# Optimization experiments

Measured on AMD Instinct MI355X. Metric: run time of the kernel, lower is better.

The kernel has to match this reference:

```python
import jax, jax.numpy as jnp
import numpy as np

EPS = 1e-5
LEAKY = 0.2


def _wn(v, g):
    # weight norm over all dims except output-channel dim 0 (torch default dim=0)
    return g * v / jnp.sqrt(jnp.sum(v * v, axis=(1, 2), keepdims=True))


def _conv1d(x_bsc, w, b):
    # x_bsc: [B,S,C_in]; w: [C_out,C_in,3]; kernel 3, stride 1, pad 1
    x = x_bsc.transpose(0, 2, 1)  # NCH
    y = jax.lax.conv_general_dilated(x, w, (1,), [(1, 1)],
                                     dimension_numbers=("NCH", "OIH", "NCH"))
    y = y + b[None, :, None]
    return y.transpose(0, 2, 1)


def _adain(x, style, lengths, proj_w, proj_b):
    # masked per-(sample,channel) instance norm over valid length, then style affine, then mask
    B, S, H = x.shape
    hs = style @ proj_w.T + proj_b            # [B, 2H]
    gamma, beta = hs[:, :H], hs[:, H:]
    mask = (jnp.arange(S)[None, :] < lengths[:, None]).astype(x.dtype)[..., None]  # [B,S,1]
    cnt = lengths.astype(x.dtype)[:, None, None]
    mean = jnp.sum(x * mask, axis=1, keepdims=True) / cnt
    var = jnp.sum(jnp.square(x - mean) * mask, axis=1, keepdims=True) / cnt  # biased, as F.instance_norm
    xn = (x - mean) * jax.lax.rsqrt(var + EPS)
    out = ((1.0 + gamma[:, None, :]) * xn + beta[:, None, :]) * mask
    return out, mask


def setup_inputs() -> dict:
    key = jax.random.key(0)
    ks = jax.random.split(key, 12)
    B, S, H, STY = 8, 2048, 512, 128
    inp = {
        "hidden_states": jax.random.normal(ks[0], (B, S, H), jnp.float32),
        "style": jax.random.normal(ks[1], (B, STY), jnp.float32),
        "input_lengths": jax.random.randint(ks[2], (B,), S // 2, S + 1, jnp.int32),
        # AdaIN projections (torch Linear: [out,in])
        "proj1_w": jax.random.normal(ks[3], (2 * H, STY), jnp.float32) * 0.02,
        "proj1_b": jnp.zeros((2 * H,), jnp.float32),
        "proj2_w": jax.random.normal(ks[4], (2 * H, STY), jnp.float32) * 0.02,
        "proj2_b": jnp.zeros((2 * H,), jnp.float32),
        # weight-normed conv1 / conv2: v [out,in,3], g [out,1,1], bias [out]
        "conv1_v": jax.random.normal(ks[5], (H, H, 3), jnp.float32) * 0.02,
        "conv1_g": jnp.ones((H, 1, 1), jnp.float32),
        "conv1_b": jnp.zeros((H,), jnp.float32),
        "conv2_v": jax.random.normal(ks[6], (H, H, 3), jnp.float32) * 0.02,
        "conv2_g": jnp.ones((H, 1, 1), jnp.float32),
        "conv2_b": jnp.zeros((H,), jnp.float32),
    }
    return inp


def reference(hidden_states, style, input_lengths,
              proj1_w, proj1_b, proj2_w, proj2_b,
              conv1_v, conv1_g, conv1_b, conv2_v, conv2_g, conv2_b):
    w1 = _wn(conv1_v, conv1_g)
    w2 = _wn(conv2_v, conv2_g)
    # residual branch
    h, mask = _adain(hidden_states, style, input_lengths, proj1_w, proj1_b)
    h = jnp.where(h >= 0, h, LEAKY * h)
    h = _conv1d(h, w1, conv1_b) * mask
    h, _ = _adain(h, style, input_lengths, proj2_w, proj2_b)
    h = jnp.where(h >= 0, h, LEAKY * h)
    h = _conv1d(h, w2, conv2_b) * mask
    # shortcut is identity (no upsample, no learned shortcut)
    return (h + hidden_states) / jnp.sqrt(jnp.asarray(2.0, hidden_states.dtype))
```

## Files before the change

### kernel.cpp

```cpp
#include <hip/hip_runtime.h>

#define NB 8
#define SS 2048
#define HH 512
#define NSTY 128
#define SP (SS + 2)
#define EPSF 1e-5f

#define BM 128
#define BN 128
#define BK 64

typedef __attribute__((ext_vector_type(8))) short short8;
typedef __attribute__((ext_vector_type(4))) float floatx4;
typedef __attribute__((ext_vector_type(4))) unsigned short u16x4;
typedef unsigned short u16;

__device__ __forceinline__ float bf2f(u16 u) {
  union { float f; unsigned int i; } v; v.i = ((unsigned int)u) << 16; return v.f;
}
__device__ __forceinline__ u16 f2bf(float f) {
  union { float f; unsigned int i; } v; v.f = f;
  unsigned int x = v.i;
  return (u16)((x + 0x7fffu + ((x >> 16) & 1u)) >> 16);
}
__device__ __forceinline__ float lrelu(float v) { return v >= 0.f ? v : 0.2f * v; }

__device__ __forceinline__ void gld_lds16(const u16* g, u16* l) {
  __builtin_amdgcn_global_load_lds((const __attribute__((address_space(1))) void*)g,
                                   (__attribute__((address_space(3))) void*)l, 16, 0, 0);
}

__global__ void k_zero(float* p, int n) {
  int i = blockIdx.x * 256 + threadIdx.x;
  if (i < n) p[i] = 0.f;
}

__global__ void k_proj(const float* style, const float* w1, const float* b1,
                       const float* w2, const float* b2,
                       float* g1, float* be1, float* g2, float* be2) {
  int idx = blockIdx.x * 256 + threadIdx.x;
  if (idx >= 2 * NB * 2 * HH) return;
  int which = idx / (NB * 2 * HH);
  int r = idx % (NB * 2 * HH);
  int b = r / (2 * HH);
  int j = r % (2 * HH);
  const float* w = which ? w2 : w1;
  const float* bias = which ? b2 : b1;
  float acc = bias[j];
  const float* st = style + b * NSTY;
  const float* wr = w + j * NSTY;
  for (int t = 0; t < NSTY; t++) acc += st[t] * wr[t];
  float* gd = which ? g2 : g1;
  float* bd = which ? be2 : be1;
  if (j < HH) gd[b * HH + j] = acc;
  else        bd[b * HH + (j - HH)] = acc;
}

__global__ void k_wnorm(const float* v1, const float* g1, const float* v2, const float* g2,
                        u16* wt1, u16* wt2) {
  int o = blockIdx.x % HH;
  int which = blockIdx.x / HH;
  const float* v = which ? v2 : v1;
  const float* g = which ? g2 : g1;
  u16* wt = which ? wt2 : wt1;
  float s = 0.f;
  for (int e = threadIdx.x; e < HH * 3; e += 256) {
    float x = v[o * HH * 3 + e];
    s += x * x;
  }
  for (int off = 32; off > 0; off >>= 1) s += __shfl_down(s, off, 64);
  __shared__ float red[4];
  int wid = threadIdx.x >> 6, lane = threadIdx.x & 63;
  if (lane == 0) red[wid] = s;
  __syncthreads();
  float tot = red[0] + red[1] + red[2] + red[3];
  float scale = g[o] / sqrtf(tot);
  for (int e = threadIdx.x; e < HH * 3; e += 256) {
    int i = e / 3, k = e % 3;
    wt[(k * HH + o) * HH + i] = f2bf(v[o * HH * 3 + e] * scale);
  }
}

#define SSPLIT1 64
__global__ void k_stats_f32(const float* __restrict__ x, const int* __restrict__ lens,
                            float* __restrict__ sum, float* __restrict__ sumsq) {
  int b = blockIdx.x & 7;
  int chunk = blockIdx.x >> 3;
  int s0 = chunk * (SS / SSPLIT1);
  int h4 = (threadIdx.x & 127) * 4;
  int sr = threadIdx.x >> 7;
  int len = lens[b];
  float4 sm = {0.f, 0.f, 0.f, 0.f}, sq = {0.f, 0.f, 0.f, 0.f};
#pragma unroll
  for (int i = 0; i < 16; i++) {
    int s = s0 + i * 2 + sr;
    float4 v = *(const float4*)(x + ((long)(b * SS + s)) * HH + h4);
    float m = (s < len) ? 1.f : 0.f;
    v.x *= m; v.y *= m; v.z *= m; v.w *= m;
    sm.x += v.x; sm.y += v.y; sm.z += v.z; sm.w += v.w;
    sq.x += v.x * v.x; sq.y += v.y * v.y; sq.z += v.z * v.z; sq.w += v.w * v.w;
  }
  atomicAdd(&sum[b * HH + h4 + 0], sm.x);
  atomicAdd(&sum[b * HH + h4 + 1], sm.y);
  atomicAdd(&sum[b * HH + h4 + 2], sm.z);
  atomicAdd(&sum[b * HH + h4 + 3], sm.w);
  atomicAdd(&sumsq[b * HH + h4 + 0], sq.x);
  atomicAdd(&sumsq[b * HH + h4 + 1], sq.y);
  atomicAdd(&sumsq[b * HH + h4 + 2], sq.z);
  atomicAdd(&sumsq[b * HH + h4 + 3], sq.w);
}

__global__ void k_fin(const float* sum, const float* sumsq, const int* lens,
                      const float* gam, const float* bet, float* a, float* c) {
  int idx = blockIdx.x * 256 + threadIdx.x;
  if (idx >= NB * HH) return;
  int b = idx / HH;
  float cnt = (float)lens[b];
  float mean = sum[idx] / cnt;
  float var = sumsq[idx] / cnt - mean * mean;
  float rs = rsqrtf(var + EPSF);
  float av = (1.f + gam[idx]) * rs;
  a[idx] = av;
  c[idx] = bet[idx] - mean * av;
}

__global__ void k_prep_f32(const float* x, const float* a, const float* c,
                           const int* lens, u16* z) {
  int b = blockIdx.x & 7;
  int v = (blockIdx.x >> 3) * 256 + threadIdx.x;
  long off = (long)v * 4;
  int i = (int)(off % HH);
  int r = (int)(off / HH);
  int s = r - 1;
  u16x4 outv;
  if (s < 0 || s >= SS || s >= lens[b]) {
    outv = (u16x4){0, 0, 0, 0};
  } else {
    const float4 xv = *(const float4*)(x + ((long)(b * SS + s)) * HH + i);
    const float4 av = *(const float4*)(a + b * HH + i);
    const float4 cv = *(const float4*)(c + b * HH + i);
    outv.x = f2bf(lrelu(av.x * xv.x + cv.x));
    outv.y = f2bf(lrelu(av.y * xv.y + cv.y));
    outv.z = f2bf(lrelu(av.z * xv.z + cv.z));
    outv.w = f2bf(lrelu(av.w * xv.w + cv.w));
  }
  *(u16x4*)(z + ((long)(b * SP + r)) * HH + i) = outv;
}

__global__ void k_prep_bf16(const u16* y, const float* a, const float* c,
                            const int* lens, u16* z) {
  int b = blockIdx.x & 7;
  int v = (blockIdx.x >> 3) * 256 + threadIdx.x;
  long off = (long)v * 4;
  int i = (int)(off % HH);
  int r = (int)(off / HH);
  int s = r - 1;
  u16x4 outv;
  if (s < 0 || s >= SS || s >= lens[b]) {
    outv = (u16x4){0, 0, 0, 0};
  } else {
    const u16x4 yv = *(const u16x4*)(y + ((long)(b * SS + s)) * HH + i);
    const float4 av = *(const float4*)(a + b * HH + i);
    const float4 cv = *(const float4*)(c + b * HH + i);
    outv.x = f2bf(lrelu(av.x * bf2f(yv.x) + cv.x));
    outv.y = f2bf(lrelu(av.y * bf2f(yv.y) + cv.y));
    outv.z = f2bf(lrelu(av.z * bf2f(yv.z) + cv.z));
    outv.w = f2bf(lrelu(av.w * bf2f(yv.w) + cv.w));
  }
  *(u16x4*)(z + ((long)(b * SP + r)) * HH + i) = outv;
}

__global__ __launch_bounds__(512, 4) void k_conv(const u16* __restrict__ z,
                                                 const u16* __restrict__ wt,
                                                 const float* __restrict__ bias,
                                                 const int* __restrict__ lens,
                                                 u16* __restrict__ yout,
                                                 const float* __restrict__ resid,
                                                 float* __restrict__ fout,
                                                 float* __restrict__ sum,
                                                 float* __restrict__ sumsq) {
  __shared__ __align__(16) u16 L[2][2][BM * BK];

  int nwg = gridDim.x;
  int bid = blockIdx.x;
  int t = (bid & 7) * (nwg >> 3) + (bid >> 3);
  int bn0 = (t % (HH / BN)) * BN; t /= (HH / BN);
  int bm0 = (t % (SS / BM)) * BM; t /= (SS / BM);
  int b = t;

  int tid = threadIdx.x;
  int wave = tid >> 6, lane = tid & 63;
  int team = wave >> 2;
  int tw = wave & 3;
  int wr = tw >> 1, wc = tw & 1;
  int l15 = lane & 15, l4 = lane >> 4;

  int t256 = tid & 255;
  int trow = t256 >> 3;
  int tslot = t256 & 7;

  u16* LA = &L[team][0][0];
  u16* LB = &L[team][1][0];

  const u16* zb = z + (size_t)b * SP * HH;
  int len = lens[b];
  int kt0 = team * 12;

  floatx4 acc[4][4] = {};

  for (int kt = 0; kt < 12; kt++) {
    int k0 = (kt0 + kt) * BK;
    const u16* wkb = wt + (size_t)(k0 >> 9) * HH * HH + (k0 & 511);
#pragma unroll
    for (int rr = 0; rr < 4; rr++) {
      int r = rr * 32 + trow;
      int sc = (tslot ^ (r & 7)) * 8;
      gld_lds16(zb + (size_t)(bm0 + r) * HH + k0 + sc, LA + rr * 2048 + t256 * 8);
    }
#pragma unroll
    for (int rr = 0; rr < 4; rr++) {
      int r = rr * 32 + trow;
      int sc = (tslot ^ (r & 7)) * 8;
      gld_lds16(wkb + (size_t)(bn0 + r) * HH + sc, LB + rr * 2048 + t256 * 8);
    }
    __syncthreads();
#pragma unroll
    for (int kk = 0; kk < 2; kk++) {
      short8 afr[4], bfr[4];
#pragma unroll
      for (int i = 0; i < 4; i++) {
        int ar = wr * 64 + i * 16 + l15;
        afr[i] = *(const short8*)&LA[ar * BK + (((kk * 4 + l4) ^ (ar & 7)) * 8)];
      }
#pragma unroll
      for (int j = 0; j < 4; j++) {
        int br = wc * 64 + j * 16 + l15;
        bfr[j] = *(const short8*)&LB[br * BK + (((kk * 4 + l4) ^ (br & 7)) * 8)];
      }
#pragma unroll
      for (int am = 0; am < 4; am++)
#pragma unroll
        for (int bn = 0; bn < 4; bn++)
          acc[am][bn] = __builtin_amdgcn_mfma_f32_16x16x32_bf16(afr[am], bfr[bn], acc[am][bn], 0, 0, 0);
    }
    __syncthreads();
  }

  floatx4* scr = (floatx4*)&L[0][0][0];
  floatx4* my = scr + (size_t)team * 2048;
  if (team == 0) {
#pragma unroll
    for (int am = 0; am < 4; am++) {
      my[(am * 2 + 0) * 256 + t256] = acc[am][2];
      my[(am * 2 + 1) * 256 + t256] = acc[am][3];
    }
  } else {
#pragma unroll
    for (int am = 0; am < 4; am++) {
      my[(am * 2 + 0) * 256 + t256] = acc[am][0];
      my[(am * 2 + 1) * 256 + t256] = acc[am][1];
    }
  }
  __syncthreads();
  const floatx4* other = scr + (size_t)(team ^ 1) * 2048;
  if (team == 0) {
#pragma unroll
    for (int am = 0; am < 4; am++) {
      acc[am][0] += other[(am * 2 + 0) * 256 + t256];
      acc[am][1] += other[(am * 2 + 1) * 256 + t256];
    }
  } else {
#pragma unroll
    for (int am = 0; am < 4; am++) {
      acc[am][2] += other[(am * 2 + 0) * 256 + t256];
      acc[am][3] += other[(am * 2 + 1) * 256 + t256];
    }
  }

#define EPI(BN) do {                                                         \
    int o = bn0 + wc * 64 + (BN) * 16 + l15;                                 \
    float bv = bias[o];                                                      \
    float psum = 0.f, psq = 0.f;                                             \
    _Pragma("unroll")                                                        \
    for (int am = 0; am < 4; am++) {                                         \
      _Pragma("unroll")                                                      \
      for (int r = 0; r < 4; r++) {                                          \
        int s = bm0 + wr * 64 + am * 16 + l4 * 4 + r;                        \
        float v = acc[am][BN][r] + bv;                                       \
        v = (s < len) ? v : 0.f;                                             \
        size_t off = ((size_t)(b * SS + s)) * HH + o;                        \
        if (fout) {                                                          \
          fout[off] = (v + resid[off]) * 0.70710678118654752f;               \
        } else {                                                             \
          yout[off] = f2bf(v);                                               \
          psum += v;                                                         \
          psq += v * v;                                                      \
        }                                                                    \
      }                                                                      \
    }                                                                        \
    if (sum) {                                                               \
      psum += __shfl_xor(psum, 16, 64);                                      \
      psum += __shfl_xor(psum, 32, 64);                                      \
      psq  += __shfl_xor(psq, 16, 64);                                       \
      psq  += __shfl_xor(psq, 32, 64);                                       \
      if (l4 == 0) {                                                         \
        atomicAdd(&sum[b * HH + o], psum);                                   \
        atomicAdd(&sumsq[b * HH + o], psq);                                  \
      }                                                                      \
    }                                                                        \
  } while (0)

  if (team == 0) { EPI(0); EPI(1); }
  else           { EPI(2); EPI(3); }
#undef EPI
}

extern "C" void kernel_launch(void* const* d_in, const int* in_sizes, int n_in,
                              void* d_out, int out_size, void* d_ws, size_t ws_size,
                              hipStream_t stream) {
  const float* x    = (const float*)d_in[0];
  const float* sty  = (const float*)d_in[1];
  const int*   lens = (const int*)d_in[2];
  const float* p1w  = (const float*)d_in[3];
  const float* p1b  = (const float*)d_in[4];
  const float* p2w  = (const float*)d_in[5];
  const float* p2b  = (const float*)d_in[6];
  const float* c1v  = (const float*)d_in[7];
  const float* c1g  = (const float*)d_in[8];
  const float* c1b  = (const float*)d_in[9];
  const float* c2v  = (const float*)d_in[10];
  const float* c2g  = (const float*)d_in[11];
  const float* c2b  = (const float*)d_in[12];
  float* out = (float*)d_out;

  char* ws = (char*)d_ws;
  size_t cur = 0;
  auto alloc = [&](size_t bytes) {
    void* p = ws + cur;
    cur += (bytes + 255) & ~(size_t)255;
    return p;
  };
  u16*   wt1  = (u16*)alloc((size_t)3 * HH * HH * 2);
  u16*   wt2  = (u16*)alloc((size_t)3 * HH * HH * 2);
  float* g1   = (float*)alloc(NB * HH * 4);
  float* be1  = (float*)alloc(NB * HH * 4);
  float* g2   = (float*)alloc(NB * HH * 4);
  float* be2  = (float*)alloc(NB * HH * 4);
  float* sum1 = (float*)alloc(NB * HH * 4);
  float* sq1  = (float*)alloc(NB * HH * 4);
  float* sum2 = (float*)alloc(NB * HH * 4);
  float* sq2  = (float*)alloc(NB * HH * 4);
  float* a1   = (float*)alloc(NB * HH * 4);
  float* c1   = (float*)alloc(NB * HH * 4);
  float* a2   = (float*)alloc(NB * HH * 4);
  float* c2   = (float*)alloc(NB * HH * 4);
  u16*   z1   = (u16*)alloc((size_t)NB * SP * HH * 2);
  u16*   y1   = (u16*)alloc((size_t)NB * SS * HH * 2);
  u16*   z2   = (u16*)alloc((size_t)NB * SP * HH * 2);

  const int CGRID = NB * (SS / BM) * (HH / BN);

  k_zero<<<(4 * NB * HH + 255) / 256, 256, 0, stream>>>(sum1, 4 * NB * HH);

  k_proj<<<(2 * NB * 2 * HH + 255) / 256, 256, 0, stream>>>(sty, p1w, p1b, p2w, p2b,
                                                            g1, be1, g2, be2);
  k_wnorm<<<2 * HH, 256, 0, stream>>>(c1v, c1g, c2v, c2g, wt1, wt2);

  k_stats_f32<<<NB * SSPLIT1, 256, 0, stream>>>(x, lens, sum1, sq1);
  k_fin<<<(NB * HH + 255) / 256, 256, 0, stream>>>(sum1, sq1, lens, g1, be1, a1, c1);

  k_prep_f32<<<NB * (SP * HH / 4 / 256), 256, 0, stream>>>(x, a1, c1, lens, z1);

  k_conv<<<CGRID, 512, 0, stream>>>(z1, wt1, c1b, lens, y1,
                                    nullptr, nullptr, sum2, sq2);

  k_fin<<<(NB * HH + 255) / 256, 256, 0, stream>>>(sum2, sq2, lens, g2, be2, a2, c2);

  k_prep_bf16<<<NB * (SP * HH / 4 / 256), 256, 0, stream>>>(y1, a2, c2, lens, z2);

  k_conv<<<CGRID, 512, 0, stream>>>(z2, wt2, c2b, lens, nullptr,
                                    x, out, nullptr, nullptr);
}
```

Before: 126.0 us.

## Double-buffer conv K-loop with async LDS loads and fold finalize into prep

The conv GEMM main loop changes from a single LDS buffer with two syncthreads per 64-wide K tile to a double-buffered 32-wide K pipeline. The next stage's global-to-LDS loads are issued before computing the current one, using vmcnt waits and raw barriers, with a new swizzled layout and raised wave priority around the MFMAs. Separately, the k_fin kernels are removed and the per-channel mean/rstd/affine computation is inlined into the prep kernels, saving two launches and the a/c buffers. The costs are redundant affine math per element and more barriers per K step.

```diff
diff --git a/kernel.cpp b/kernel.cpp
--- a/kernel.cpp
+++ b/kernel.cpp
@@ -9,7 +9,6 @@
 
 #define BM 128
 #define BN 128
-#define BK 64
 
 typedef __attribute__((ext_vector_type(8))) short short8;
 typedef __attribute__((ext_vector_type(4))) float floatx4;
@@ -111,35 +110,44 @@
   atomicAdd(&sumsq[b * HH + h4 + 3], sq.w);
 }
 
-__global__ void k_fin(const float* sum, const float* sumsq, const int* lens,
-                      const float* gam, const float* bet, float* a, float* c) {
-  int idx = blockIdx.x * 256 + threadIdx.x;
-  if (idx >= NB * HH) return;
-  int b = idx / HH;
-  float cnt = (float)lens[b];
-  float mean = sum[idx] / cnt;
-  float var = sumsq[idx] / cnt - mean * mean;
-  float rs = rsqrtf(var + EPSF);
-  float av = (1.f + gam[idx]) * rs;
-  a[idx] = av;
-  c[idx] = bet[idx] - mean * av;
-}
-
-__global__ void k_prep_f32(const float* x, const float* a, const float* c,
-                           const int* lens, u16* z) {
+__device__ __forceinline__ void affine4(const float* sum, const float* sumsq,
+                                        const float* gam, const float* bet,
+                                        int b, int i, float cnt,
+                                        float4& av, float4& cv) {
+  float4 sm = *(const float4*)(sum + b * HH + i);
+  float4 sq = *(const float4*)(sumsq + b * HH + i);
+  float4 gv = *(const float4*)(gam + b * HH + i);
+  float4 bv = *(const float4*)(bet + b * HH + i);
+  float rc = 1.f / cnt;
+  float mx = sm.x * rc, my = sm.y * rc, mz = sm.z * rc, mw = sm.w * rc;
+  av.x = (1.f + gv.x) * rsqrtf(sq.x * rc - mx * mx + EPSF);
+  av.y = (1.f + gv.y) * rsqrtf(sq.y * rc - my * my + EPSF);
+  av.z = (1.f + gv.z) * rsqrtf(sq.z * rc - mz * mz + EPSF);
+  av.w = (1.f + gv.w) * rsqrtf(sq.w * rc - mw * mw + EPSF);
+  cv.x = bv.x - mx * av.x;
+  cv.y = bv.y - my * av.y;
+  cv.z = bv.z - mz * av.z;
+  cv.w = bv.w - mw * av.w;
+}
+
+__global__ void k_prep_f32(const float* __restrict__ x,
+                           const float* __restrict__ sum, const float* __restrict__ sumsq,
+                           const float* __restrict__ gam, const float* __restrict__ bet,
+                           const int* __restrict__ lens, u16* __restrict__ z) {
   int b = blockIdx.x & 7;
   int v = (blockIdx.x >> 3) * 256 + threadIdx.x;
   long off = (long)v * 4;
   int i = (int)(off % HH);
   int r = (int)(off / HH);
   int s = r - 1;
+  int len = lens[b];
   u16x4 outv;
-  if (s < 0 || s >= SS || s >= lens[b]) {
+  if (s < 0 || s >= SS || s >= len) {
     outv = (u16x4){0, 0, 0, 0};
   } else {
+    float4 av, cv;
+    affine4(sum, sumsq, gam, bet, b, i, (float)len, av, cv);
     const float4 xv = *(const float4*)(x + ((long)(b * SS + s)) * HH + i);
-    const float4 av = *(const float4*)(a + b * HH + i);
-    const float4 cv = *(const float4*)(c + b * HH + i);
     outv.x = f2bf(lrelu(av.x * xv.x + cv.x));
     outv.y = f2bf(lrelu(av.y * xv.y + cv.y));
     outv.z = f2bf(lrelu(av.z * xv.z + cv.z));
@@ -148,21 +156,24 @@
   *(u16x4*)(z + ((long)(b * SP + r)) * HH + i) = outv;
 }
 
-__global__ void k_prep_bf16(const u16* y, const float* a, const float* c,
-                            const int* lens, u16* z) {
+__global__ void k_prep_bf16(const u16* __restrict__ y,
+                            const float* __restrict__ sum, const float* __restrict__ sumsq,
+                            const float* __restrict__ gam, const float* __restrict__ bet,
+                            const int* __restrict__ lens, u16* __restrict__ z) {
   int b = blockIdx.x & 7;
   int v = (blockIdx.x >> 3) * 256 + threadIdx.x;
   long off = (long)v * 4;
   int i = (int)(off % HH);
   int r = (int)(off / HH);
   int s = r - 1;
+  int len = lens[b];
   u16x4 outv;
-  if (s < 0 || s >= SS || s >= lens[b]) {
+  if (s < 0 || s >= SS || s >= len) {
     outv = (u16x4){0, 0, 0, 0};
   } else {
+    float4 av, cv;
+    affine4(sum, sumsq, gam, bet, b, i, (float)len, av, cv);
     const u16x4 yv = *(const u16x4*)(y + ((long)(b * SS + s)) * HH + i);
-    const float4 av = *(const float4*)(a + b * HH + i);
-    const float4 cv = *(const float4*)(c + b * HH + i);
     outv.x = f2bf(lrelu(av.x * bf2f(yv.x) + cv.x));
     outv.y = f2bf(lrelu(av.y * bf2f(yv.y) + cv.y));
     outv.z = f2bf(lrelu(av.z * bf2f(yv.z) + cv.z));
@@ -180,7 +191,7 @@
                                                  float* __restrict__ fout,
                                                  float* __restrict__ sum,
                                                  float* __restrict__ sumsq) {
-  __shared__ __align__(16) u16 L[2][2][BM * BK];
+  __shared__ __align__(16) u16 L[2][2][2][BM * 32];
 
   int nwg = gridDim.x;
   int bid = blockIdx.x;
@@ -197,57 +208,80 @@
   int l15 = lane & 15, l4 = lane >> 4;
 
   int t256 = tid & 255;
-  int trow = t256 >> 3;
-  int tslot = t256 & 7;
-
-  u16* LA = &L[team][0][0];
-  u16* LB = &L[team][1][0];
+
+  u16* A0 = &L[team][0][0][0];
+  u16* B0 = &L[team][0][1][0];
+  u16* A1 = &L[team][1][0][0];
+  u16* B1 = &L[team][1][1][0];
 
   const u16* zb = z + (size_t)b * SP * HH;
   int len = lens[b];
-  int kt0 = team * 12;
 
   floatx4 acc[4][4] = {};
 
-  for (int kt = 0; kt < 12; kt++) {
-    int k0 = (kt0 + kt) * BK;
+  auto stage = [&](u16* dA, u16* dB, int st) {
+    int k0 = st * 32;
     const u16* wkb = wt + (size_t)(k0 >> 9) * HH * HH + (k0 & 511);
 #pragma unroll
-    for (int rr = 0; rr < 4; rr++) {
-      int r = rr * 32 + trow;
-      int sc = (tslot ^ (r & 7)) * 8;
-      gld_lds16(zb + (size_t)(bm0 + r) * HH + k0 + sc, LA + rr * 2048 + t256 * 8);
-    }
-#pragma unroll
-    for (int rr = 0; rr < 4; rr++) {
-      int r = rr * 32 + trow;
-      int sc = (tslot ^ (r & 7)) * 8;
-      gld_lds16(wkb + (size_t)(bn0 + r) * HH + sc, LB + rr * 2048 + t256 * 8);
-    }
-    __syncthreads();
-#pragma unroll
-    for (int kk = 0; kk < 2; kk++) {
-      short8 afr[4], bfr[4];
-#pragma unroll
-      for (int i = 0; i < 4; i++) {
-        int ar = wr * 64 + i * 16 + l15;
-        afr[i] = *(const short8*)&LA[ar * BK + (((kk * 4 + l4) ^ (ar & 7)) * 8)];
-      }
-#pragma unroll
-      for (int j = 0; j < 4; j++) {
-        int br = wc * 64 + j * 16 + l15;
-        bfr[j] = *(const short8*)&LB[br * BK + (((kk * 4 + l4) ^ (br & 7)) * 8)];
-      }
-#pragma unroll
-      for (int am = 0; am < 4; am++)
-#pragma unroll
-        for (int bn = 0; bn < 4; bn++)
-          acc[am][bn] = __builtin_amdgcn_mfma_f32_16x16x32_bf16(afr[am], bfr[bn], acc[am][bn], 0, 0, 0);
-    }
-    __syncthreads();
-  }
-
-  floatx4* scr = (floatx4*)&L[0][0][0];
+    for (int i = 0; i < 2; i++) {
+      int g = i * 256 + t256;
+      int line = g >> 3, pp = g & 7;
+      int p = pp ^ (line & 7);
+      int r = line * 2 + (p >> 2), s = p & 3;
+      gld_lds16(zb + (size_t)(bm0 + r) * HH + k0 + s * 8, dA + g * 8);
+    }
+#pragma unroll
+    for (int i = 0; i < 2; i++) {
+      int g = i * 256 + t256;
+      int line = g >> 3, pp = g & 7;
+      int p = pp ^ (line & 7);
+      int r = line * 2 + (p >> 2), s = p & 3;
+      gld_lds16(wkb + (size_t)(bn0 + r) * HH + s * 8, dB + g * 8);
+    }
+  };
+
+  auto compute = [&](const u16* sA, const u16* sB) {
+    short8 afr[4], bfr[4];
+#pragma unroll
+    for (int i = 0; i < 4; i++) {
+      int ar = wr * 64 + i * 16 + l15;
+      afr[i] = *(const short8*)&sA[(ar >> 1) * 64 + ((((ar & 1) * 4 + l4) ^ ((ar >> 1) & 7)) * 8)];
+    }
+#pragma unroll
+    for (int j = 0; j < 4; j++) {
+      int br = wc * 64 + j * 16 + l15;
+      bfr[j] = *(const short8*)&sB[(br >> 1) * 64 + ((((br & 1) * 4 + l4) ^ ((br >> 1) & 7)) * 8)];
+    }
+    __builtin_amdgcn_s_setprio(1);
+#pragma unroll
+    for (int am = 0; am < 4; am++)
+#pragma unroll
+      for (int bn = 0; bn < 4; bn++)
+        acc[am][bn] = __builtin_amdgcn_mfma_f32_16x16x32_bf16(afr[am], bfr[bn], acc[am][bn], 0, 0, 0);
+    __builtin_amdgcn_s_setprio(0);
+  };
+
+  int st0 = team * 24;
+  stage(A0, B0, st0);
+  for (int tp = 0; tp < 12; tp++) {
+    stage(A1, B1, st0 + 2 * tp + 1);
+    asm volatile("s_waitcnt vmcnt(4)" ::: "memory");
+    __builtin_amdgcn_s_barrier();
+    compute(A0, B0);
+    __builtin_amdgcn_s_barrier();
+    if (tp < 11) {
+      stage(A0, B0, st0 + 2 * tp + 2);
+      asm volatile("s_waitcnt vmcnt(4)" ::: "memory");
+    } else {
+      asm volatile("s_waitcnt vmcnt(0)" ::: "memory");
+    }
+    __builtin_amdgcn_s_barrier();
+    compute(A1, B1);
+    if (tp < 11) __builtin_amdgcn_s_barrier();
+  }
+  __syncthreads();
+
+  floatx4* scr = (floatx4*)&L[0][0][0][0];
   floatx4* my = scr + (size_t)team * 2048;
   if (team == 0) {
 #pragma unroll
@@ -351,10 +385,6 @@
   float* sq1  = (float*)alloc(NB * HH * 4);
   float* sum2 = (float*)alloc(NB * HH * 4);
   float* sq2  = (float*)alloc(NB * HH * 4);
-  float* a1   = (float*)alloc(NB * HH * 4);
-  float* c1   = (float*)alloc(NB * HH * 4);
-  float* a2   = (float*)alloc(NB * HH * 4);
-  float* c2   = (float*)alloc(NB * HH * 4);
   u16*   z1   = (u16*)alloc((size_t)NB * SP * HH * 2);
   u16*   y1   = (u16*)alloc((size_t)NB * SS * HH * 2);
   u16*   z2   = (u16*)alloc((size_t)NB * SP * HH * 2);
@@ -368,16 +398,15 @@
   k_wnorm<<<2 * HH, 256, 0, stream>>>(c1v, c1g, c2v, c2g, wt1, wt2);
 
   k_stats_f32<<<NB * SSPLIT1, 256, 0, stream>>>(x, lens, sum1, sq1);
-  k_fin<<<(NB * HH + 255) / 256, 256, 0, stream>>>(sum1, sq1, lens, g1, be1, a1, c1);
-
-  k_prep_f32<<<NB * (SP * HH / 4 / 256), 256, 0, stream>>>(x, a1, c1, lens, z1);
+
+  k_prep_f32<<<NB * (SP * HH / 4 / 256), 256, 0, stream>>>(x, sum1, sq1, g1, be1,
+                                                           lens, z1);
 
   k_conv<<<CGRID, 512, 0, stream>>>(z1, wt1, c1b, lens, y1,
                                     nullptr, nullptr, sum2, sq2);
 
-  k_fin<<<(NB * HH + 255) / 256, 256, 0, stream>>>(sum2, sq2, lens, g2, be2, a2, c2);
-
-  k_prep_bf16<<<NB * (SP * HH / 4 / 256), 256, 0, stream>>>(y1, a2, c2, lens, z2);
+  k_prep_bf16<<<NB * (SP * HH / 4 / 256), 256, 0, stream>>>(y1, sum2, sq2, g2, be2,
+                                                            lens, z2);
 
   k_conv<<<CGRID, 512, 0, stream>>>(z2, wt2, c2b, lens, nullptr,
                                     x, out, nullptr, nullptr);
```

New measurement: 133.9 us. 1.06x slower.
